# Optimization experiments

Measured on AMD Instinct MI355X. Metric: run time of the kernel, lower is better.

## Reference

```python
import math
import jax, jax.numpy as jnp
import numpy as np

STEP = 0.1
EPS = 1e-12


def _laplacian(src, dst, n):
    # dense symmetric-normalized Laplacian from COO edge list (symmetrized, 0/1 weights)
    A = jnp.zeros((n, n), dtype=jnp.float32).at[src, dst].set(1.0)
    A = jnp.maximum(A, A.T)
    deg = A.sum(axis=1)
    dinv = jnp.where(deg > 0, 1.0 / jnp.sqrt(jnp.maximum(deg, 1e-12)), 0.0)
    return jnp.eye(n, dtype=jnp.float32) - dinv[:, None] * A * dinv[None, :]


def _filter_bank(L, bs):
    # rational band-pass bank centered at b in arange(0,2.1,STEP):
    # D_b = sqrt(2)*a * inv((L - b I)^4 + a I),  a = (STEP/2)^4
    n = L.shape[0]
    a = (STEP / 2.0) ** 4
    I = jnp.eye(n, dtype=L.dtype)

    def one(b):
        M1 = L - b * I
        P2 = M1 @ M1
        P4 = P2 @ P2
        return math.sqrt(2.0) * a * jnp.linalg.inv(P4 + a * I)

    return jax.vmap(one)(bs)  # [F, n, n]


def _cdist_mean(e):
    # mean pairwise euclidean distance, safe sqrt on the zero diagonal
    d2 = jnp.sum((e[:, None, :] - e[None, :, :]) ** 2, axis=-1)
    d = jnp.sqrt(jnp.where(d2 > 0, d2, 1.0))
    return jnp.where(d2 > 0, d, 0.0).mean()


def setup_inputs() -> dict:
    key = jax.random.key(0)
    k1, k2, k3, k4, k5 = jax.random.split(key, 5)
    B, N, F0, R, E = 64, 128, 32, 1118, 512
    return {
        "x": jax.random.normal(k1, (B, N, F0), dtype=jnp.float32),
        "random_signal": jax.random.normal(k2, (B, N, R), dtype=jnp.float32),
        "C": jax.random.normal(k3, (21, 1), dtype=jnp.float32),
        "edge_src": jax.random.randint(k4, (B, E), 0, N),
        "edge_dst": jax.random.randint(k5, (B, E), 0, N),
        "num_classes": 4,
    }


def reference(x, random_signal, C, edge_src, edge_dst, num_classes):
    B, N, _ = x.shape
    R = random_signal.shape[-1]
    # torch.normal(0, sqrt(1/R)) random signal concatenated to features
    feats = jnp.concatenate([x, random_signal * math.sqrt(1.0 / R)], axis=-1)  # [B,N,F0+R]
    bs = jnp.arange(0.0, 2.1, STEP, dtype=jnp.float32)  # [21]
    Cn = C / jnp.maximum(jnp.linalg.norm(C, axis=0, keepdims=True), EPS)  # F.normalize(C, dim=0)

    def per_graph(src, dst, xg):
        L = _laplacian(src, dst, N)
        D = _filter_bank(L, bs)                      # [F,N,N]
        L_hat = jnp.einsum('fnm,f->nm', D, Cn[:, 0])  # D.permute(1,2,0) @ C, squeezed
        A_hat = jnp.eye(N, dtype=xg.dtype) - L_hat
        y = A_hat @ xg                                # [N, F0+R]
        z = y / jnp.maximum(jnp.linalg.norm(y, axis=1, keepdims=True), EPS)
        logits = z @ z.T                              # decode_all on normalized x
        sp = -jnp.abs(logits).sum() / (N * N)         # -||logits||_1 / n^2
        return y.mean(axis=0), sp

    emb, sp_terms = jax.vmap(per_graph)(edge_src, edge_dst, feats)  # [B,D], [B]

    # faithful repeated in-loop division: s_{i+1} = (s_i + t_i)/B  =>  sum_i t_i * B^{-(B-i)}
    i = jnp.arange(B, dtype=jnp.float32)
    w = jnp.exp(-(B - i) * jnp.log(float(B)))
    sparsity_fwd = jnp.sum(sp_terms * w)

    # labels y = arange(B) % num_classes; one positive group (class members) and
    # one negative group (non-members) per class
    idx = np.arange(B)
    hl1 = jnp.float32(0.0)
    hl2 = jnp.float32(0.0)
    for c in range(num_classes):
        pos = jnp.asarray(idx[idx % num_classes == c])
        neg = jnp.asarray(idx[idx % num_classes != c])
        beta = 1.0 / num_classes + 1e-13  # one group per class
        hl1 = hl1 + (-_cdist_mean(emb[neg])) / beta
        hl2 = hl2 + _cdist_mean(emb[pos])

    Fk = C.shape[0]
    dims = jnp.sqrt(jnp.float32(Fk))
    c_l1 = jnp.sum(jnp.abs(C), axis=0)
    c_l2 = jnp.maximum(jnp.linalg.norm(C, axis=0), EPS)
    sparsity_c = jnp.mean((dims - c_l1 / c_l2) / (dims - 1.0))

    return sparsity_c + hl2 + hl1 + sparsity_fwd
```

## Files before the change

### kernel.cpp

```cpp
#include <hip/hip_runtime.h>
#include <math.h>

#define NN 128
#define SM 129
#define TS 132
#define RS 132
#define SS 17
#define SF 132
#define XS 68
#define YS 132

typedef double d4 __attribute__((ext_vector_type(4)));

__global__ __launch_bounds__(256) void k1_lap(
    const int* __restrict__ src, const int* __restrict__ dst,
    int E, float* __restrict__ Lout) {
  extern __shared__ float sm1[];
  float* A    = sm1;
  float* dinv = sm1 + NN * SM;
  const int g   = blockIdx.x;
  const int tid = threadIdx.x;

  for (int e = tid; e < NN * NN; e += 256) {
    int i = e >> 7, j = e & 127;
    A[i * SM + j] = 0.f;
  }
  __syncthreads();
  const int* s = src + (size_t)g * E;
  const int* d = dst + (size_t)g * E;
  for (int e = tid; e < E; e += 256) {
    int a = s[e], b = d[e];
    A[a * SM + b] = 1.f;
    A[b * SM + a] = 1.f;
  }
  __syncthreads();
  if (tid < NN) {
    float acc = 0.f;
    for (int j = 0; j < NN; ++j) acc += A[tid * SM + j];
    dinv[tid] = (acc > 0.f) ? (float)(1.0 / sqrt((double)acc)) : 0.f;
  }
  __syncthreads();
  float* Lg = Lout + (size_t)g * NN * NN;
  for (int e = tid; e < NN * NN; e += 256) {
    int i = e >> 7, j = e & 127;
    Lg[e] = ((i == j) ? 1.f : 0.f) - dinv[i] * dinv[j] * A[i * SM + j];
  }
}

__global__ __launch_bounds__(512, 4) void kpow2(
    const float* __restrict__ L, double* __restrict__ L2) {
  extern __shared__ float Bs[];
  const int bid = blockIdx.x;
  const int g = bid >> 3, q = bid & 7;
  const int tid = threadIdx.x;
  const int wv = tid >> 6, ln = tid & 63;
  const int m  = ln & 15, kq = ln >> 4;
  const int rb = 16 * q;
  const int cb = wv;

  int rIdx[4], cIdx[4];
  {
    d4 z = {0.0, 0.0, 0.0, 0.0};
    d4 pr = __builtin_amdgcn_mfma_f64_16x16x4f64((double)m, 1.0, z, 0, 0, 0);
    d4 pc = __builtin_amdgcn_mfma_f64_16x16x4f64(1.0, (double)m, z, 0, 0, 0);
#pragma unroll
    for (int r = 0; r < 4; ++r) {
      rIdx[r] = ((int)(pr[r] * 0.25 + 0.5)) & 15;
      cIdx[r] = ((int)(pc[r] * 0.25 + 0.5)) & 15;
    }
  }

  const float* Lg = L + (size_t)g * NN * NN;
  for (int e4 = tid; e4 < (NN * NN) / 4; e4 += 512) {
    int i = e4 >> 5, j4 = (e4 & 31) * 4;
    *(float4*)(Bs + i * SF + j4) = *(const float4*)(Lg + i * NN + j4);
  }
  __syncthreads();

  d4 acc = {0.0, 0.0, 0.0, 0.0};
  for (int kc = 0; kc < 32; ++kc) {
    double a = (double)Bs[(rb + m) * SF + 4 * kc + kq];
    double b = (double)Bs[(4 * kc + kq) * SF + 16 * cb + m];
    acc = __builtin_amdgcn_mfma_f64_16x16x4f64(a, b, acc, 0, 0, 0);
  }
  double* out = L2 + (size_t)g * NN * NN;
#pragma unroll
  for (int r = 0; r < 4; ++r)
    out[(rb + rIdx[r]) * NN + 16 * cb + cIdx[r]] = acc[r];
}

__global__ __launch_bounds__(512, 4) void kpow34(
    const float* __restrict__ L, const double* __restrict__ L2,
    double* __restrict__ L3, double* __restrict__ L4) {
  extern __shared__ float Bs[];
  const int bid = blockIdx.x;
  const int g = bid >> 3, q = (bid >> 1) & 3, job = bid & 1;
  const int tid = threadIdx.x;
  const int wv = tid >> 6, ln = tid & 63;
  const int m  = ln & 15, kq = ln >> 4;
  const int rb = 32 * q + 16 * (wv & 1);
  const int cb0 = 2 * (wv >> 1);

  int rIdx[4], cIdx[4];
  {
    d4 z = {0.0, 0.0, 0.0, 0.0};
    d4 pr = __builtin_amdgcn_mfma_f64_16x16x4f64((double)m, 1.0, z, 0, 0, 0);
    d4 pc = __builtin_amdgcn_mfma_f64_16x16x4f64(1.0, (double)m, z, 0, 0, 0);
#pragma unroll
    for (int r = 0; r < 4; ++r) {
      rIdx[r] = ((int)(pr[r] * 0.25 + 0.5)) & 15;
      cIdx[r] = ((int)(pc[r] * 0.25 + 0.5)) & 15;
    }
  }

  const float*  Lg  = L  + (size_t)g * NN * NN;
  const double* L2g = L2 + (size_t)g * NN * NN;
  if (job == 0) {
    for (int e4 = tid; e4 < (NN * NN) / 4; e4 += 512) {
      int i = e4 >> 5, j4 = (e4 & 31) * 4;
      *(float4*)(Bs + i * SF + j4) = *(const float4*)(Lg + i * NN + j4);
    }
  }
  __syncthreads();

  d4 acc[2];
#pragma unroll
  for (int c = 0; c < 2; ++c) {
    acc[c][0] = 0.0; acc[c][1] = 0.0; acc[c][2] = 0.0; acc[c][3] = 0.0;
  }
  if (job == 0) {
    for (int kc = 0; kc < 32; ++kc) {
      double a = L2g[(rb + m) * NN + 4 * kc + kq];
#pragma unroll
      for (int c = 0; c < 2; ++c) {
        double b = (double)Bs[(4 * kc + kq) * SF + 16 * (cb0 + c) + m];
        acc[c] = __builtin_amdgcn_mfma_f64_16x16x4f64(a, b, acc[c], 0, 0, 0);
      }
    }
  } else {
    for (int kc = 0; kc < 32; ++kc) {
      double a = L2g[(rb + m) * NN + 4 * kc + kq];
#pragma unroll
      for (int c = 0; c < 2; ++c) {
        double b = L2g[(4 * kc + kq) * NN + 16 * (cb0 + c) + m];
        acc[c] = __builtin_amdgcn_mfma_f64_16x16x4f64(a, b, acc[c], 0, 0, 0);
      }
    }
  }
  double* out = (job == 0 ? L3 : L4) + (size_t)g * NN * NN;
#pragma unroll
  for (int c = 0; c < 2; ++c)
#pragma unroll
    for (int r = 0; r < 4; ++r)
      out[(rb + rIdx[r]) * NN + 16 * (cb0 + c) + cIdx[r]] = acc[c][r];
}

__global__ __launch_bounds__(512, 4) void k2_filter(
    const float* __restrict__ L, const double* __restrict__ L2,
    const double* __restrict__ L3, const double* __restrict__ L4,
    const float* __restrict__ C, int NF, float* __restrict__ W) {
  extern __shared__ char smraw[];
  double* Rp  = (double*)smraw;
  double* Scd = (double*)(smraw + 16 * RS * 8);
  double* Pv  = (double*)(smraw + 16 * RS * 8 + 8 * 16 * SS * 8);

  const int bid = blockIdx.x;
  const int g = bid / NF, f = bid % NF;
  const int tid = threadIdx.x;
  const int wv = tid >> 6, ln = tid & 63;
  const int m  = ln & 15, kq = ln >> 4;
  double* S = Scd + wv * 16 * SS;

  double csum = 0.0;
  for (int q = 0; q < NF; ++q) { double c = (double)C[q]; csum += c * c; }
  double cn = sqrt(csum); if (cn < 1e-12) cn = 1e-12;
  const double a4 = 6.25e-6;
  const double coef = 1.4142135623730951 * a4 * ((double)C[f] / cn);
  const float  bf = (float)((double)f * 0.1);
  const double bb = (double)bf;
  const double c3 = -4.0 * bb;
  const double c2 = 6.0 * bb * bb;
  const double c1 = -4.0 * bb * bb * bb;
  const double c0 = bb * bb * bb * bb + a4;

  int rIdx[4], cIdx[4];
  {
    d4 z = {0.0, 0.0, 0.0, 0.0};
    d4 pr = __builtin_amdgcn_mfma_f64_16x16x4f64((double)m, 1.0, z, 0, 0, 0);
    d4 pc = __builtin_amdgcn_mfma_f64_16x16x4f64(1.0, (double)m, z, 0, 0, 0);
#pragma unroll
    for (int r = 0; r < 4; ++r) {
      rIdx[r] = ((int)(pr[r] * 0.25 + 0.5)) & 15;
      cIdx[r] = ((int)(pc[r] * 0.25 + 0.5)) & 15;
    }
  }

  const float*  Lg  = L  + (size_t)g * NN * NN;
  const double* L2g = L2 + (size_t)g * NN * NN;
  const double* L3g = L3 + (size_t)g * NN * NN;
  const double* L4g = L4 + (size_t)g * NN * NN;
  d4 T[8];
#pragma unroll
  for (int cb = 0; cb < 8; ++cb)
#pragma unroll
    for (int r = 0; r < 4; ++r) {
      int i = 16 * wv + rIdx[r], j = 16 * cb + cIdx[r];
      int idx = i * NN + j;
      double v = L4g[idx];
      v = fma(c3, L3g[idx], v);
      v = fma(c2, L2g[idx], v);
      v = fma(c1, (double)Lg[idx], v);
      if (i == j) v += c0;
      T[cb][r] = v;
    }

#pragma unroll 1
  for (int t = 0; t < 8; ++t) {
    if (wv == t) {
#pragma unroll
      for (int cb = 0; cb < 8; ++cb)
#pragma unroll
        for (int r = 0; r < 4; ++r)
          Rp[rIdx[r] * RS + 16 * cb + cIdx[r]] = T[cb][r];
    }
    __syncthreads();

    if (wv == t) {
      double sr[4];
#pragma unroll
      for (int r = 0; r < 4; ++r) sr[r] = Rp[(4 * r + kq) * RS + 16 * t + m];
#pragma unroll
      for (int k = 0; k < 16; ++k) {
        const int kr = k >> 2, kl = k & 3;
        double pv   = __shfl(sr[kr], 16 * kl + k);
        double rowv = __shfl(sr[kr], 16 * kl + m);
        double cv[4];
#pragma unroll
        for (int r = 0; r < 4; ++r) cv[r] = __shfl(sr[r], 16 * kq + k);
        double dp = 1.0 / pv;
#pragma unroll
        for (int r = 0; r < 4; ++r) {
          int i = 4 * r + kq;
          double nv;
          if (i == k)      nv = (m == k) ? dp : rowv * dp;
          else if (m == k) nv = -cv[r] * dp;
          else             nv = fma(-(cv[r] * dp), rowv, sr[r]);
          sr[r] = nv;
        }
      }
#pragma unroll
      for (int r = 0; r < 4; ++r) Pv[(4 * r + kq) * SS + m] = sr[r];
    }
    __syncthreads();

#pragma unroll
    for (int cb = 0; cb < 8; ++cb) {
      if (cb != t) continue;
      if (wv == t) {
#pragma unroll
        for (int r = 0; r < 4; ++r) T[cb][r] = Pv[rIdx[r] * SS + cIdx[r]];
      } else {
#pragma unroll
        for (int r = 0; r < 4; ++r) S[rIdx[r] * SS + cIdx[r]] = T[cb][r];
        __builtin_amdgcn_wave_barrier();
        d4 ncv = {0.0, 0.0, 0.0, 0.0};
#pragma unroll
        for (int kc = 0; kc < 4; ++kc) {
          double a = S[m * SS + 4 * kc + kq];
          double b = -Pv[(4 * kc + kq) * SS + m];
          ncv = __builtin_amdgcn_mfma_f64_16x16x4f64(a, b, ncv, 0, 0, 0);
        }
        T[cb] = ncv;
        __builtin_amdgcn_wave_barrier();
#pragma unroll
        for (int r = 0; r < 4; ++r) S[rIdx[r] * SS + cIdx[r]] = T[cb][r];
      }
    }
    __builtin_amdgcn_wave_barrier();

    const double* asrc = (wv == t) ? Pv : S;
#pragma unroll
    for (int cb = 0; cb < 8; ++cb) {
      if (cb == t) continue;
      d4 acc;
      if (wv == t) { acc[0] = 0.0; acc[1] = 0.0; acc[2] = 0.0; acc[3] = 0.0; }
      else         { acc = T[cb]; }
#pragma unroll
      for (int kc = 0; kc < 4; ++kc) {
        double a = asrc[m * SS + 4 * kc + kq];
        double b = Rp[(4 * kc + kq) * RS + 16 * cb + m];
        acc = __builtin_amdgcn_mfma_f64_16x16x4f64(a, b, acc, 0, 0, 0);
      }
      T[cb] = acc;
    }
    __syncthreads();
  }

  float* Wg = W + (size_t)g * NN * NN;
#pragma unroll
  for (int cb = 0; cb < 8; ++cb)
#pragma unroll
    for (int r = 0; r < 4; ++r)
      atomicAdd(&Wg[(16 * wv + rIdx[r]) * NN + 16 * cb + cIdx[r]],
                (float)(coef * T[cb][r]));
}

__global__ __launch_bounds__(512, 8) void k3_fused64(
    const float* __restrict__ x, const float* __restrict__ rs,
    const float* __restrict__ W, float* __restrict__ Gp,
    float* __restrict__ emb, int F0, int R, int DTOT, int NCH2,
    float rscale) {
  extern __shared__ float sm3[];
  float* ldsX = sm3;
  float* embA = sm3 + 128 * XS;
  const int bid = blockIdx.x;
  const int g = bid / NCH2;
  const int c = bid % NCH2;
  const int d0 = c * 64;
  const int tid = threadIdx.x, tr = tid >> 4, tc = tid & 15;

  const float* xg = x + (size_t)g * NN * F0;
  const float* rg = rs + (size_t)g * NN * R;
  for (int e = tid; e < NN * 64; e += 512) {
    int k = e >> 6, dl = e & 63;
    int d = d0 + dl;
    float v = 0.f;
    if (d < DTOT) v = (d < F0) ? xg[k * F0 + d] : rg[k * R + (d - F0)] * rscale;
    ldsX[k * XS + dl] = v;
  }
  if (tid < 64) embA[tid] = 0.f;
  __syncthreads();

  const float* Wg = W + (size_t)g * NN * NN;
  float acc[4][4];
#pragma unroll
  for (int v = 0; v < 4; ++v)
#pragma unroll
    for (int u = 0; u < 4; ++u) acc[v][u] = 0.f;
  float4 w4 = *(const float4*)(Wg + 4 * tr);
  for (int k = 0; k < NN; ++k) {
    float4 w4n;
    if (k < NN - 1) w4n = *(const float4*)(Wg + (k + 1) * NN + 4 * tr);
    float4 xa = *(const float4*)(ldsX + k * XS + 4 * tc);
    float xv[4] = {xa.x, xa.y, xa.z, xa.w};
    float wvv[4] = {w4.x, w4.y, w4.z, w4.w};
#pragma unroll
    for (int v = 0; v < 4; ++v)
#pragma unroll
      for (int u = 0; u < 4; ++u) acc[v][u] = fmaf(wvv[v], xv[u], acc[v][u]);
    w4 = w4n;
  }
#pragma unroll
  for (int v = 0; v < 4; ++v) {
    float4 sa = *(const float4*)(ldsX + (4 * tr + v) * XS + 4 * tc);
    acc[v][0] = sa.x - acc[v][0]; acc[v][1] = sa.y - acc[v][1];
    acc[v][2] = sa.z - acc[v][2]; acc[v][3] = sa.w - acc[v][3];
  }

#pragma unroll
  for (int u = 0; u < 4; ++u) {
    float s = acc[0][u] + acc[1][u] + acc[2][u] + acc[3][u];
    atomicAdd(&embA[4 * tc + u], s);
  }
  __syncthreads();

#pragma unroll
  for (int v = 0; v < 4; ++v)
#pragma unroll
    for (int u = 0; u < 4; ++u)
      ldsX[(4 * tc + u) * YS + 4 * tr + v] = acc[v][u];
  __syncthreads();

  if (tid < 64) {
    int d = d0 + tid;
    if (d < DTOT) emb[(size_t)g * 1152 + d] = embA[tid] * (1.f / 128.f);
  }

  float gg[4][8];
#pragma unroll
  for (int v = 0; v < 4; ++v)
#pragma unroll
    for (int u = 0; u < 8; ++u) gg[v][u] = 0.f;
  for (int dl = 0; dl < 64; ++dl) {
    float4 a4v = *(const float4*)(ldsX + dl * YS + 4 * tr);
    float4 ba  = *(const float4*)(ldsX + dl * YS + 4 * tc);
    float4 bb  = *(const float4*)(ldsX + dl * YS + 64 + 4 * tc);
    float bv[8] = {ba.x, ba.y, ba.z, ba.w, bb.x, bb.y, bb.z, bb.w};
    float av[4] = {a4v.x, a4v.y, a4v.z, a4v.w};
#pragma unroll
    for (int v = 0; v < 4; ++v)
#pragma unroll
      for (int u = 0; u < 8; ++u) gg[v][u] = fmaf(av[v], bv[u], gg[v][u]);
  }
  float* Gc = Gp + ((size_t)c * 64 + g) * NN * NN;
#pragma unroll
  for (int v = 0; v < 4; ++v) {
    float4 lo = {gg[v][0], gg[v][1], gg[v][2], gg[v][3]};
    float4 hi = {gg[v][4], gg[v][5], gg[v][6], gg[v][7]};
    *(float4*)(Gc + (4 * tr + v) * NN + 4 * tc) = lo;
    *(float4*)(Gc + (4 * tr + v) * NN + 64 + 4 * tc) = hi;
  }
}

__global__ __launch_bounds__(256) void kgred(
    const float* __restrict__ Gp, float* __restrict__ G, int NCH) {
  const size_t cstride = (size_t)64 * NN * NN;
  size_t idx = ((size_t)blockIdx.x * 256 + threadIdx.x) * 4;
  float4 s = *(const float4*)(Gp + idx);
  for (int c = 1; c < NCH; ++c) {
    float4 v = *(const float4*)(Gp + c * cstride + idx);
    s.x += v.x; s.y += v.y; s.z += v.z; s.w += v.w;
  }
  *(float4*)(G + idx) = s;
}

__global__ __launch_bounds__(256) void k45_fused(
    const float* __restrict__ G, double* __restrict__ spt,
    const float* __restrict__ emb, float* __restrict__ Dm, int DTOT) {
  __shared__ float inr[NN];
  __shared__ double red[4];
  const int bid = blockIdx.x, tid = threadIdx.x;
  if (bid < 256) {
    const int g = bid >> 2, qt = bid & 3;
    const float* Gg = G + (size_t)g * NN * NN;
    if (tid < NN) {
      float n = sqrtf(fmaxf(Gg[tid * NN + tid], 0.f));
      inr[tid] = 1.f / fmaxf(n, 1e-12f);
    }
    __syncthreads();
    double s = 0.0;
    const int base = qt * 4096;
    for (int e0 = tid; e0 < 4096; e0 += 256) {
      int e = base + e0;
      int i = e >> 7, j = e & 127;
      s += (double)(fabsf(Gg[e]) * inr[i] * inr[j]);
    }
    for (int off = 32; off; off >>= 1) s += __shfl_down(s, off);
    int wave = tid >> 6, lane = tid & 63;
    if (lane == 0) red[wave] = s;
    __syncthreads();
    if (tid == 0) atomicAdd(&spt[g], red[0] + red[1] + red[2] + red[3]);
  } else {
    const int ii = bid - 256;
    const int i = ii >> 1, h = ii & 1;
    const int wv = tid >> 6, l = tid & 63;
    float ei[18];
#pragma unroll
    for (int s = 0; s < 18; ++s) {
      int d = l + 64 * s;
      ei[s] = (d < DTOT) ? emb[(size_t)i * 1152 + d] : 0.f;
    }
    for (int jj = 8 * h; jj < 8 * h + 8; ++jj) {
      int j = 4 * jj + wv;
      float acc = 0.f;
#pragma unroll
      for (int s = 0; s < 18; ++s) {
        int d = l + 64 * s;
        if (d < DTOT) {
          float df = ei[s] - emb[(size_t)j * 1152 + d];
          acc = fmaf(df, df, acc);
        }
      }
      for (int off = 32; off; off >>= 1) acc += __shfl_down(acc, off);
      if (l == 0) Dm[i * 64 + j] = (acc > 0.f) ? sqrtf(acc) : 0.f;
    }
  }
}

__global__ __launch_bounds__(256) void k5b_final(
    const float* __restrict__ Dm, const double* __restrict__ spt,
    const float* __restrict__ C, int NF,
    const int* __restrict__ ncls, float* __restrict__ out) {
  __shared__ double redH[8];
  __shared__ double redS;
  const int tid = threadIdx.x;
  const int wv = tid >> 6, lane = tid & 63;
  const int nc = ncls[0];

  double hl1 = 0.0, hl2 = 0.0;
  const double beta = 1.0 / (double)nc + 1e-13;
  for (int cc = wv; cc < nc; cc += 4) {
    bool ip = (lane % nc) == cc;
    double ps = 0.0, ns = 0.0;
    for (int j = 0; j < 64; ++j) {
      double dv = (double)Dm[lane * 64 + j];
      bool jp = (j % nc) == cc;
      if (ip && jp) ps += dv;
      if (!ip && !jp) ns += dv;
    }
    for (int off = 32; off; off >>= 1) {
      ps += __shfl_down(ps, off);
      ns += __shfl_down(ns, off);
    }
    if (lane == 0) {
      int npos = 0;
      for (int q = 0; q < 64; ++q) if (q % nc == cc) npos++;
      int nneg = 64 - npos;
      hl2 += ps / ((double)npos * (double)npos);
      hl1 += -(ns / ((double)nneg * (double)nneg)) / beta;
    }
  }
  if (lane == 0) { redH[2 * wv] = hl1; redH[2 * wv + 1] = hl2; }

  if (wv == 0) {
    double sp = -spt[lane] * (1.0 / (double)(NN * NN));
    double spf = sp * exp(-((double)(64 - lane)) * log(64.0));
    for (int off = 32; off; off >>= 1) spf += __shfl_down(spf, off);
    if (lane == 0) redS = spf;
  }
  __syncthreads();

  if (tid == 0) {
    double h1 = redH[0] + redH[2] + redH[4] + redH[6];
    double h2 = redH[1] + redH[3] + redH[5] + redH[7];
    double l1 = 0.0, l2 = 0.0;
    for (int q = 0; q < NF; ++q) { double cv = (double)C[q]; l1 += fabs(cv); l2 += cv * cv; }
    l2 = sqrt(l2); if (l2 < 1e-12) l2 = 1e-12;
    double dims = sqrt((double)NF);
    double sc = (dims - l1 / l2) / (dims - 1.0);
    out[0] = (float)(sc + h2 + h1 + redS);
  }
}

extern "C" void kernel_launch(void* const* d_in, const int* in_sizes, int n_in,
                              void* d_out, int out_size, void* d_ws, size_t ws_size,
                              hipStream_t stream) {
  (void)n_in; (void)out_size;
  const float* x    = (const float*)d_in[0];
  const float* rs   = (const float*)d_in[1];
  const float* C    = (const float*)d_in[2];
  const int*   esrc = (const int*)d_in[3];
  const int*   edst = (const int*)d_in[4];
  const int*   ncls = (const int*)d_in[5];
  float* out = (float*)d_out;

  const int F0   = in_sizes[0] / (64 * 128);
  const int R    = in_sizes[1] / (64 * 128);
  const int NF   = in_sizes[2];
  const int E    = in_sizes[3] / 64;
  const int DTOT = F0 + R;
  const int NCH  = (DTOT + 127) / 128;
  const int NCH2 = (DTOT + 63) / 64;
  const float rscale = (float)(1.0 / sqrt((double)R));
  (void)NCH;

  char* ws = (char*)d_ws;
  size_t off = 0;
  float*  L    = (float*)(ws + off);  off += (size_t)64 * NN * NN * 4;
  float*  W    = (float*)(ws + off);  off += (size_t)64 * NN * NN * 4;
  float*  Gp   = (float*)(ws + off);
  double* L2d  = (double*)(ws + off); off += (size_t)64 * NN * NN * 8;
  double* L3d  = (double*)(ws + off); off += (size_t)64 * NN * NN * 8;
  double* L4d  = (double*)(ws + off); off += (size_t)64 * NN * NN * 8;
  {
    size_t gp_bytes = (size_t)NCH2 * 64 * NN * NN * 4;
    size_t have = (size_t)3 * 64 * NN * NN * 8;
    if (gp_bytes > have) off += gp_bytes - have;
  }
  float*  emb  = (float*)(ws + off);  off += (size_t)64 * 1152 * 4;
  double* spt  = (double*)(ws + off); off += (size_t)64 * 8;
  float*  Dm   = (float*)(ws + off);  off += (size_t)64 * 64 * 4;
  float*  G    = L;

  hipMemsetAsync(W, 0, (size_t)64 * NN * NN * 4, stream);
  hipMemsetAsync(spt, 0, (size_t)64 * 8, stream);

  const int lds1 = (NN * SM + NN) * 4;
  const int ldsf = NN * SF * 4;
  const int lds2 = 16 * RS * 8 + 8 * 16 * SS * 8 + 16 * SS * 8;
  const int lds364 = (128 * XS + 64) * 4;
  hipFuncSetAttribute((const void*)k1_lap,    hipFuncAttributeMaxDynamicSharedMemorySize, lds1);
  hipFuncSetAttribute((const void*)kpow2,     hipFuncAttributeMaxDynamicSharedMemorySize, ldsf);
  hipFuncSetAttribute((const void*)kpow34,    hipFuncAttributeMaxDynamicSharedMemorySize, ldsf);
  hipFuncSetAttribute((const void*)k2_filter, hipFuncAttributeMaxDynamicSharedMemorySize, lds2);
  hipFuncSetAttribute((const void*)k3_fused64, hipFuncAttributeMaxDynamicSharedMemorySize, lds364);

  k1_lap<<<64, 256, lds1, stream>>>(esrc, edst, E, L);
  kpow2<<<512, 512, ldsf, stream>>>(L, L2d);
  kpow34<<<512, 512, ldsf, stream>>>(L, L2d, L3d, L4d);
  k2_filter<<<64 * NF, 512, lds2, stream>>>(L, L2d, L3d, L4d, C, NF, W);
  k3_fused64<<<64 * NCH2, 512, lds364, stream>>>(x, rs, W, Gp, emb, F0, R, DTOT, NCH2, rscale);
  kgred<<<1024, 256, 0, stream>>>(Gp, G, NCH2);
  k45_fused<<<384, 256, 0, stream>>>(G, spt, emb, Dm, DTOT);
  k5b_final<<<1, 256, 0, stream>>>(Dm, spt, C, NF, ncls, out);
}
```

Before: 537.8 us.

## Double-buffer pivot panels in filter inversion to cut block barriers per step

The blocked Gauss-Jordan inversion in the filter kernel now keeps two copies of the pivot row panel and pivot block in LDS, alternating between them on each step. The pivot wave writes the row panel and inverts the 16x16 pivot block before the first barrier, which removes two of the three __syncthreads per step. Doubling these buffers raises LDS use, and the launch-bounds occupancy hint drops from 4 to 2 blocks, which may lower occupancy and latency hiding.

```diff
diff --git a/kernel.cpp b/kernel.cpp
--- a/kernel.cpp
+++ b/kernel.cpp
@@ -155,14 +155,38 @@
       out[(rb + rIdx[r]) * NN + 16 * (cb0 + c) + cIdx[r]] = acc[c][r];
 }
 
-__global__ __launch_bounds__(512, 4) void k2_filter(
+__device__ __forceinline__ void gj16(double sr[4], int m, int kq) {
+#pragma unroll
+  for (int k = 0; k < 16; ++k) {
+    const int kr = k >> 2, kl = k & 3;
+    double pv   = __shfl(sr[kr], 16 * kl + k);
+    double rowv = __shfl(sr[kr], 16 * kl + m);
+    double cv[4];
+#pragma unroll
+    for (int r = 0; r < 4; ++r) cv[r] = __shfl(sr[r], 16 * kq + k);
+    double dp = 1.0 / pv;
+#pragma unroll
+    for (int r = 0; r < 4; ++r) {
+      int i = 4 * r + kq;
+      double nv;
+      if (i == k)      nv = (m == k) ? dp : rowv * dp;
+      else if (m == k) nv = -cv[r] * dp;
+      else             nv = fma(-(cv[r] * dp), rowv, sr[r]);
+      sr[r] = nv;
+    }
+  }
+}
+
+__global__ __launch_bounds__(512, 2) void k2_filter(
     const float* __restrict__ L, const double* __restrict__ L2,
     const double* __restrict__ L3, const double* __restrict__ L4,
     const float* __restrict__ C, int NF, float* __restrict__ W) {
   extern __shared__ char smraw[];
-  double* Rp  = (double*)smraw;
-  double* Scd = (double*)(smraw + 16 * RS * 8);
-  double* Pv  = (double*)(smraw + 16 * RS * 8 + 8 * 16 * SS * 8);
+  double* Rp0 = (double*)smraw;
+  double* Rp1 = Rp0 + 16 * RS;
+  double* Scd = Rp1 + 16 * RS;
+  double* Pv0 = Scd + 8 * 16 * SS;
+  double* Pv1 = Pv0 + 16 * SS;
 
   const int bid = blockIdx.x;
   const int g = bid / NF, f = bid % NF;
@@ -216,69 +240,47 @@
 
 #pragma unroll 1
   for (int t = 0; t < 8; ++t) {
+    double* Rc = (t & 1) ? Rp1 : Rp0;
+    double* Pc = (t & 1) ? Pv1 : Pv0;
+
     if (wv == t) {
 #pragma unroll
       for (int cb = 0; cb < 8; ++cb)
 #pragma unroll
         for (int r = 0; r < 4; ++r)
-          Rp[rIdx[r] * RS + 16 * cb + cIdx[r]] = T[cb][r];
+          Rc[rIdx[r] * RS + 16 * cb + cIdx[r]] = T[cb][r];
+      __builtin_amdgcn_wave_barrier();
+      double sr[4];
+#pragma unroll
+      for (int r = 0; r < 4; ++r) sr[r] = Rc[(4 * r + kq) * RS + 16 * t + m];
+      gj16(sr, m, kq);
+#pragma unroll
+      for (int r = 0; r < 4; ++r) Pc[(4 * r + kq) * SS + m] = sr[r];
     }
     __syncthreads();
 
     if (wv == t) {
-      double sr[4];
-#pragma unroll
-      for (int r = 0; r < 4; ++r) sr[r] = Rp[(4 * r + kq) * RS + 16 * t + m];
-#pragma unroll
-      for (int k = 0; k < 16; ++k) {
-        const int kr = k >> 2, kl = k & 3;
-        double pv   = __shfl(sr[kr], 16 * kl + k);
-        double rowv = __shfl(sr[kr], 16 * kl + m);
-        double cv[4];
-#pragma unroll
-        for (int r = 0; r < 4; ++r) cv[r] = __shfl(sr[r], 16 * kq + k);
-        double dp = 1.0 / pv;
-#pragma unroll
-        for (int r = 0; r < 4; ++r) {
-          int i = 4 * r + kq;
-          double nv;
-          if (i == k)      nv = (m == k) ? dp : rowv * dp;
-          else if (m == k) nv = -cv[r] * dp;
-          else             nv = fma(-(cv[r] * dp), rowv, sr[r]);
-          sr[r] = nv;
-        }
+#pragma unroll
+      for (int r = 0; r < 4; ++r) T[t][r] = Pc[rIdx[r] * SS + cIdx[r]];
+    } else {
+#pragma unroll
+      for (int r = 0; r < 4; ++r) S[rIdx[r] * SS + cIdx[r]] = T[t][r];
+      __builtin_amdgcn_wave_barrier();
+      d4 ncv = {0.0, 0.0, 0.0, 0.0};
+#pragma unroll
+      for (int kc = 0; kc < 4; ++kc) {
+        double a = S[m * SS + 4 * kc + kq];
+        double b = -Pc[(4 * kc + kq) * SS + m];
+        ncv = __builtin_amdgcn_mfma_f64_16x16x4f64(a, b, ncv, 0, 0, 0);
       }
-#pragma unroll
-      for (int r = 0; r < 4; ++r) Pv[(4 * r + kq) * SS + m] = sr[r];
-    }
-    __syncthreads();
-
-#pragma unroll
-    for (int cb = 0; cb < 8; ++cb) {
-      if (cb != t) continue;
-      if (wv == t) {
-#pragma unroll
-        for (int r = 0; r < 4; ++r) T[cb][r] = Pv[rIdx[r] * SS + cIdx[r]];
-      } else {
-#pragma unroll
-        for (int r = 0; r < 4; ++r) S[rIdx[r] * SS + cIdx[r]] = T[cb][r];
-        __builtin_amdgcn_wave_barrier();
-        d4 ncv = {0.0, 0.0, 0.0, 0.0};
-#pragma unroll
-        for (int kc = 0; kc < 4; ++kc) {
-          double a = S[m * SS + 4 * kc + kq];
-          double b = -Pv[(4 * kc + kq) * SS + m];
-          ncv = __builtin_amdgcn_mfma_f64_16x16x4f64(a, b, ncv, 0, 0, 0);
-        }
-        T[cb] = ncv;
-        __builtin_amdgcn_wave_barrier();
-#pragma unroll
-        for (int r = 0; r < 4; ++r) S[rIdx[r] * SS + cIdx[r]] = T[cb][r];
-      }
+      T[t] = ncv;
+      __builtin_amdgcn_wave_barrier();
+#pragma unroll
+      for (int r = 0; r < 4; ++r) S[rIdx[r] * SS + cIdx[r]] = T[t][r];
     }
     __builtin_amdgcn_wave_barrier();
 
-    const double* asrc = (wv == t) ? Pv : S;
+    const double* asrc = (wv == t) ? Pc : S;
 #pragma unroll
     for (int cb = 0; cb < 8; ++cb) {
       if (cb == t) continue;
@@ -288,12 +290,11 @@
 #pragma unroll
       for (int kc = 0; kc < 4; ++kc) {
         double a = asrc[m * SS + 4 * kc + kq];
-        double b = Rp[(4 * kc + kq) * RS + 16 * cb + m];
+        double b = Rc[(4 * kc + kq) * RS + 16 * cb + m];
         acc = __builtin_amdgcn_mfma_f64_16x16x4f64(a, b, acc, 0, 0, 0);
       }
       T[cb] = acc;
     }
-    __syncthreads();
   }
 
   float* Wg = W + (size_t)g * NN * NN;
@@ -539,10 +540,8 @@
   const int NF   = in_sizes[2];
   const int E    = in_sizes[3] / 64;
   const int DTOT = F0 + R;
-  const int NCH  = (DTOT + 127) / 128;
   const int NCH2 = (DTOT + 63) / 64;
   const float rscale = (float)(1.0 / sqrt((double)R));
-  (void)NCH;
 
   char* ws = (char*)d_ws;
   size_t off = 0;
@@ -567,7 +566,7 @@
 
   const int lds1 = (NN * SM + NN) * 4;
   const int ldsf = NN * SF * 4;
-  const int lds2 = 16 * RS * 8 + 8 * 16 * SS * 8 + 16 * SS * 8;
+  const int lds2 = 2 * 16 * RS * 8 + 8 * 16 * SS * 8 + 2 * 16 * SS * 8;
   const int lds364 = (128 * XS + 64) * 4;
   hipFuncSetAttribute((const void*)k1_lap,    hipFuncAttributeMaxDynamicSharedMemorySize, lds1);
   hipFuncSetAttribute((const void*)kpow2,     hipFuncAttributeMaxDynamicSharedMemorySize, ldsf);
```

Result: slower. 873.3 us (+62.4%).
